# Performance work log

Measured on AMD Instinct MI355X. Metric: run time of the kernel, lower is better.

The kernel has to match this reference:

```python
import jax, jax.numpy as jnp
import numpy as np

PIECES = 64  # self.plane


def _proj(f, w1, b1, w2, b2):
    # Projection: fc2(relu(fc1(f))), final_relu=False
    h = jax.nn.relu(f @ w1 + b1)
    return h @ w2 + b2


def _cf(img, param, pieces):
    # img: [B,3,H,W], param: [B,3,P]
    # total[b,c,h,w] = sum_i clamp(img - i/P, 0, 1/P) * param[b,c,i], then * P / sum_i param
    grid = jnp.arange(pieces, dtype=img.dtype) / pieces            # [P]
    clipped = jnp.clip(img[..., None] - grid, 0.0, 1.0 / pieces)   # [B,3,H,W,P]
    total = jnp.einsum('bchwp,bcp->bchw', clipped, param)
    norm = pieces / (jnp.sum(param, axis=-1) + 1e-30)              # [B,3]
    return total * norm[:, :, None, None]


def setup_inputs() -> dict:
    key = jax.random.key(0)
    ks = jax.random.split(key, 11)
    B, H, W = 8, 256, 256
    s = 0.05
    return {
        'x': jax.random.uniform(ks[0], (B, 3, H, W), jnp.float32),
        'f_feature': jax.random.normal(ks[1], (B, 512), jnp.float32),
        'b_feature': jax.random.normal(ks[2], (B, 512), jnp.float32),
        # stacked weights for [fc_f_1, fc_b_1, fc_f_s, fc_b_s]
        'proj_w1': jax.random.normal(ks[3], (4, 512, 192), jnp.float32) * s,
        'proj_b1': jax.random.normal(ks[4], (4, 192), jnp.float32) * s,
        'proj_w2': jax.random.normal(ks[5], (4, 192, 192), jnp.float32) * s,
        'proj_b2': jax.random.normal(ks[6], (4, 192), jnp.float32) * s,
        'fc_w1': jax.random.normal(ks[7], (576, 192), jnp.float32) * s,
        'fc_b1': jax.random.normal(ks[8], (192,), jnp.float32) * s,
        'fc_w2': jax.random.normal(ks[9], (192, 192), jnp.float32) * s,
        'fc_b2': jax.random.normal(ks[10], (192,), jnp.float32) * s,
    }


def reference(x, f_feature, b_feature, proj_w1, proj_b1, proj_w2, proj_b2,
              fc_w1, fc_b1, fc_w2, fc_b2):
    B = x.shape[0]
    # rgb_to_grayscale with 3 output channels (ITU-R 601 weights)
    gw = jnp.array([0.299, 0.587, 0.114], dtype=x.dtype)
    gray = jnp.broadcast_to(jnp.einsum('bchw,c->bhw', x, gw)[:, None], x.shape)

    # four stacked Projections: inputs [f, b, f, b]
    feats = jnp.stack([f_feature, b_feature, f_feature, b_feature])       # [4,B,512]
    h = jax.nn.relu(jnp.einsum('kbi,kio->kbo', feats, proj_w1) + proj_b1[:, None, :])
    outs = jnp.einsum('kbo,koq->kbq', h, proj_w2) + proj_b2[:, None, :]   # [4,B,192]
    param_f, param_b = outs[0], outs[1]
    param_s = outs[2] + outs[3]

    cat = jnp.concatenate([param_f, param_b, param_s], axis=1)            # [B,576]
    param = _proj(cat, fc_w1, fc_b1, fc_w2, fc_b2)                        # [B,192]

    p_all = param.reshape(B, 3, PIECES)
    p_f = param_f.reshape(B, 3, PIECES)
    p_b = param_b.reshape(B, 3, PIECES)

    return (_cf(x, p_all, PIECES), _cf(gray, p_f, PIECES), _cf(gray, p_b, PIECES))
```

## Files before the change

### kernel.cpp

```cpp
#include <hip/hip_runtime.h>

#define HWSZ 65536
#define PLANE (3 * HWSZ)
#define OUTSTRIDE (8 * PLANE)
#define MAGIC 0x13572468

__global__ __launch_bounds__(384) void k_fused(
    const float* __restrict__ f, const float* __restrict__ bf,
    const float* __restrict__ pw1, const float* __restrict__ pb1,
    const float* __restrict__ pw2, const float* __restrict__ pb2,
    const float* __restrict__ fw1, const float* __restrict__ fb1,
    const float* __restrict__ fw2, const float* __restrict__ fb2,
    const float* __restrict__ x, float* __restrict__ out,
    float* __restrict__ ws) {
  __shared__ float smem[2304];
  int t = threadIdx.x, blk = blockIdx.x;

  float* outs  = ws;
  float* param = ws + 6144;
  int* flags = (int*)(ws + 8192);

  if (blk < 32) {
    int k = blk >> 3, b = blk & 7;
    int q = t % 48, s = t / 48;
    float* sf  = smem;
    float* red = smem + 512;
    float* sh  = smem + 2048;

    const float* feat = ((k & 1) ? bf : f) + b * 512;
    for (int i = t; i < 512; i += 384) sf[i] = feat[i];
    __syncthreads();

    {
      const float4* w = (const float4*)(pw1 + (size_t)k * (512 * 192));
      float4 acc = {0.f, 0.f, 0.f, 0.f};
      int i0 = s * 64;
      for (int r = 0; r < 4; ++r) {
        float4 wv[16];
#pragma unroll
        for (int j = 0; j < 16; ++j)
          wv[j] = w[(size_t)(i0 + r * 16 + j) * 48 + q];
#pragma unroll
        for (int j = 0; j < 16; ++j) {
          float v = sf[i0 + r * 16 + j];
          acc.x = fmaf(v, wv[j].x, acc.x); acc.y = fmaf(v, wv[j].y, acc.y);
          acc.z = fmaf(v, wv[j].z, acc.z); acc.w = fmaf(v, wv[j].w, acc.w);
        }
      }
      ((float4*)(red + s * 192))[q] = acc;
    }
    __syncthreads();
    if (t < 192) {
      float a = pb1[k * 192 + t];
#pragma unroll
      for (int s2 = 0; s2 < 8; ++s2) a += red[s2 * 192 + t];
      sh[t] = fmaxf(a, 0.f);
    }
    __syncthreads();
    {
      const float4* w = (const float4*)(pw2 + (size_t)k * (192 * 192));
      float4 acc = {0.f, 0.f, 0.f, 0.f};
      int i0 = s * 24;
      for (int r = 0; r < 2; ++r) {
        float4 wv[12];
#pragma unroll
        for (int j = 0; j < 12; ++j)
          wv[j] = w[(size_t)(i0 + r * 12 + j) * 48 + q];
#pragma unroll
        for (int j = 0; j < 12; ++j) {
          float v = sh[i0 + r * 12 + j];
          acc.x = fmaf(v, wv[j].x, acc.x); acc.y = fmaf(v, wv[j].y, acc.y);
          acc.z = fmaf(v, wv[j].z, acc.z); acc.w = fmaf(v, wv[j].w, acc.w);
        }
      }
      ((float4*)(red + s * 192))[q] = acc;
    }
    __syncthreads();
    if (t < 192) {
      float a = pb2[k * 192 + t];
#pragma unroll
      for (int s2 = 0; s2 < 8; ++s2) a += red[s2 * 192 + t];
      outs[(k * 8 + b) * 192 + t] = a;
    }
    __syncthreads();
    if (t == 0) {
      __threadfence();
      atomicExch(&flags[(k * 8 + b) * 16], MAGIC);
    }

    if (blk >= 8) return;

    int b2_ = blk;
    if (t < 4) {
      while (atomicAdd(&flags[(t * 8 + b2_) * 16], 0) != MAGIC)
        __builtin_amdgcn_s_sleep(2);
    }
    __syncthreads();
    if (t == 0) __threadfence();
    __syncthreads();

    float* sc   = smem;
    float* redb = smem + 576;
    float* shb  = smem + 2112;
    for (int idx = t; idx < 576; idx += 384) {
      float v;
      if (idx < 192)      v = outs[(0 * 8 + b2_) * 192 + idx];
      else if (idx < 384) v = outs[(1 * 8 + b2_) * 192 + (idx - 192)];
      else                v = outs[(2 * 8 + b2_) * 192 + (idx - 384)] +
                              outs[(3 * 8 + b2_) * 192 + (idx - 384)];
      sc[idx] = v;
    }
    __syncthreads();
    {
      int q = t % 48, s = t / 48;
      {
        const float4* w = (const float4*)fw1;
        float4 acc = {0.f, 0.f, 0.f, 0.f};
        int i0 = s * 72;
        for (int r = 0; r < 4; ++r) {
          float4 wv[18];
#pragma unroll
          for (int j = 0; j < 18; ++j)
            wv[j] = w[(size_t)(i0 + r * 18 + j) * 48 + q];
#pragma unroll
          for (int j = 0; j < 18; ++j) {
            float v = sc[i0 + r * 18 + j];
            acc.x = fmaf(v, wv[j].x, acc.x); acc.y = fmaf(v, wv[j].y, acc.y);
            acc.z = fmaf(v, wv[j].z, acc.z); acc.w = fmaf(v, wv[j].w, acc.w);
          }
        }
        ((float4*)(redb + s * 192))[q] = acc;
      }
      __syncthreads();
      if (t < 192) {
        float a = fb1[t];
#pragma unroll
        for (int s2 = 0; s2 < 8; ++s2) a += redb[s2 * 192 + t];
        shb[t] = fmaxf(a, 0.f);
      }
      __syncthreads();
      {
        const float4* w = (const float4*)fw2;
        float4 acc = {0.f, 0.f, 0.f, 0.f};
        int i0 = s * 24;
        for (int r = 0; r < 2; ++r) {
          float4 wv[12];
#pragma unroll
          for (int j = 0; j < 12; ++j)
            wv[j] = w[(size_t)(i0 + r * 12 + j) * 48 + q];
#pragma unroll
          for (int j = 0; j < 12; ++j) {
            float v = shb[i0 + r * 12 + j];
            acc.x = fmaf(v, wv[j].x, acc.x); acc.y = fmaf(v, wv[j].y, acc.y);
            acc.z = fmaf(v, wv[j].z, acc.z); acc.w = fmaf(v, wv[j].w, acc.w);
          }
        }
        ((float4*)(redb + s * 192))[q] = acc;
      }
      __syncthreads();
      if (t < 192) {
        float a = fb2[t];
#pragma unroll
        for (int s2 = 0; s2 < 8; ++s2) a += redb[s2 * 192 + t];
        param[b2_ * 192 + t] = a;
      }
    }
    __syncthreads();
    if (t == 0) {
      __threadfence();
      atomicExch(&flags[(32 + b2_) * 16], MAGIC);
    }
    return;
  }

  int rblk = blk - 32;
  int b = rblk / 43, chunk = rblk - b * 43;
  int s4 = chunk * 384 + t;
  bool act = s4 < (HWSZ / 4);

  const float* xb = x + (size_t)b * PLANE;
  float4 vr = {0,0,0,0}, vg = {0,0,0,0}, vb = {0,0,0,0};
  if (act) {
    vr = ((const float4*)(xb))[s4];
    vg = ((const float4*)(xb + HWSZ))[s4];
    vb = ((const float4*)(xb + 2 * HWSZ))[s4];
  }

  if (t == 0) {
    while (atomicAdd(&flags[(32 + b) * 16], 0) != MAGIC)
      __builtin_amdgcn_s_sleep(2);
    __threadfence();
  }
  __syncthreads();

  float2* tab = (float2*)smem;
  {
    int wave = t >> 6, lane = t & 63;
    for (int cur = wave; cur < 9; cur += 6) {
      int oi = cur / 3, c = cur - oi * 3;
      const float* src = (oi == 0) ? param + b * 192 + c * 64
                                   : outs + ((oi - 1) * 8 + b) * 192 + c * 64;
      float p = src[lane];
      float v = p;
#pragma unroll
      for (int d = 1; d < 64; d <<= 1) {
        float n = __shfl_up(v, d, 64);
        if (lane >= d) v += n;
      }
      float total = __shfl(v, 63, 64);
      float norm = 64.f / (total + 1e-30f);
      tab[cur * 64 + lane] = make_float2((v - p) * 0.015625f * norm, p * norm);
    }
  }
  __syncthreads();

  if (!act) return;

  auto ev = [&](int cur, float v) -> float {
    int k = (int)(v * 64.f);
    k = k < 0 ? 0 : (k > 63 ? 63 : k);
    float2 e = tab[cur * 64 + k];
    float tt = v - (float)k * 0.015625f;
    return fmaf(tt, e.y, e.x);
  };
  auto ev4 = [&](int cur, float4 v) -> float4 {
    float4 r;
    r.x = ev(cur, v.x); r.y = ev(cur, v.y);
    r.z = ev(cur, v.z); r.w = ev(cur, v.w);
    return r;
  };

  float4 gr;
  gr.x = fmaf(0.299f, vr.x, fmaf(0.587f, vg.x, 0.114f * vb.x));
  gr.y = fmaf(0.299f, vr.y, fmaf(0.587f, vg.y, 0.114f * vb.y));
  gr.z = fmaf(0.299f, vr.z, fmaf(0.587f, vg.z, 0.114f * vb.z));
  gr.w = fmaf(0.299f, vr.w, fmaf(0.587f, vg.w, 0.114f * vb.w));

  float* o0 = out + (size_t)b * PLANE;
  float* o1 = out + OUTSTRIDE + (size_t)b * PLANE;
  float* o2 = out + 2 * OUTSTRIDE + (size_t)b * PLANE;

  ((float4*)(o0))[s4]            = ev4(0, vr);
  ((float4*)(o0 + HWSZ))[s4]     = ev4(1, vg);
  ((float4*)(o0 + 2 * HWSZ))[s4] = ev4(2, vb);
  ((float4*)(o1))[s4]            = ev4(3, gr);
  ((float4*)(o1 + HWSZ))[s4]     = ev4(4, gr);
  ((float4*)(o1 + 2 * HWSZ))[s4] = ev4(5, gr);
  ((float4*)(o2))[s4]            = ev4(6, gr);
  ((float4*)(o2 + HWSZ))[s4]     = ev4(7, gr);
  ((float4*)(o2 + 2 * HWSZ))[s4] = ev4(8, gr);
}

extern "C" void kernel_launch(void* const* d_in, const int* in_sizes, int n_in,
                              void* d_out, int out_size, void* d_ws, size_t ws_size,
                              hipStream_t stream) {
  const float* x   = (const float*)d_in[0];
  const float* f   = (const float*)d_in[1];
  const float* bf  = (const float*)d_in[2];
  const float* pw1 = (const float*)d_in[3];
  const float* pb1 = (const float*)d_in[4];
  const float* pw2 = (const float*)d_in[5];
  const float* pb2 = (const float*)d_in[6];
  const float* fw1 = (const float*)d_in[7];
  const float* fb1 = (const float*)d_in[8];
  const float* fw2 = (const float*)d_in[9];
  const float* fb2 = (const float*)d_in[10];
  float* out = (float*)d_out;
  float* ws  = (float*)d_ws;

  k_fused<<<376, 384, 0, stream>>>(f, bf, pw1, pb1, pw2, pb2, fw1, fb1, fw2,
                                   fb2, x, out, ws);
}
```

Before: 108.6 us.

## Split fused kernel into MLP kernel and separate render kernel

The single persistent kernel is split in two. The first computes the projection MLPs (32 blocks, keeping the intra-kernel flag wait for the final fc stage), and the second renders the curve outputs over a 64x8 grid of 256-thread blocks. This removes the spin-wait of render blocks on the per-batch param flags and relies on stream ordering instead. In exchange it adds a second launch, and the loads of x can no longer overlap with the MLP computation.

```diff
diff --git a/kernel.cpp b/kernel.cpp
--- a/kernel.cpp
+++ b/kernel.cpp
@@ -5,13 +5,12 @@
 #define OUTSTRIDE (8 * PLANE)
 #define MAGIC 0x13572468
 
-__global__ __launch_bounds__(384) void k_fused(
+__global__ __launch_bounds__(384) void k_mlp(
     const float* __restrict__ f, const float* __restrict__ bf,
     const float* __restrict__ pw1, const float* __restrict__ pb1,
     const float* __restrict__ pw2, const float* __restrict__ pb2,
     const float* __restrict__ fw1, const float* __restrict__ fb1,
     const float* __restrict__ fw2, const float* __restrict__ fb2,
-    const float* __restrict__ x, float* __restrict__ out,
     float* __restrict__ ws) {
   __shared__ float smem[2304];
   int t = threadIdx.x, blk = blockIdx.x;
@@ -20,9 +19,9 @@
   float* param = ws + 6144;
   int* flags = (int*)(ws + 8192);
 
-  if (blk < 32) {
-    int k = blk >> 3, b = blk & 7;
-    int q = t % 48, s = t / 48;
+  int k = blk >> 3, b = blk & 7;
+  int q = t % 48, s = t / 48;
+  {
     float* sf  = smem;
     float* red = smem + 512;
     float* sh  = smem + 2048;
@@ -87,134 +86,109 @@
       __threadfence();
       atomicExch(&flags[(k * 8 + b) * 16], MAGIC);
     }
-
-    if (blk >= 8) return;
-
-    int b2_ = blk;
-    if (t < 4) {
-      while (atomicAdd(&flags[(t * 8 + b2_) * 16], 0) != MAGIC)
-        __builtin_amdgcn_s_sleep(2);
-    }
-    __syncthreads();
-    if (t == 0) __threadfence();
-    __syncthreads();
-
-    float* sc   = smem;
-    float* redb = smem + 576;
-    float* shb  = smem + 2112;
-    for (int idx = t; idx < 576; idx += 384) {
-      float v;
-      if (idx < 192)      v = outs[(0 * 8 + b2_) * 192 + idx];
-      else if (idx < 384) v = outs[(1 * 8 + b2_) * 192 + (idx - 192)];
-      else                v = outs[(2 * 8 + b2_) * 192 + (idx - 384)] +
-                              outs[(3 * 8 + b2_) * 192 + (idx - 384)];
-      sc[idx] = v;
-    }
-    __syncthreads();
-    {
-      int q = t % 48, s = t / 48;
-      {
-        const float4* w = (const float4*)fw1;
-        float4 acc = {0.f, 0.f, 0.f, 0.f};
-        int i0 = s * 72;
-        for (int r = 0; r < 4; ++r) {
-          float4 wv[18];
-#pragma unroll
-          for (int j = 0; j < 18; ++j)
-            wv[j] = w[(size_t)(i0 + r * 18 + j) * 48 + q];
-#pragma unroll
-          for (int j = 0; j < 18; ++j) {
-            float v = sc[i0 + r * 18 + j];
-            acc.x = fmaf(v, wv[j].x, acc.x); acc.y = fmaf(v, wv[j].y, acc.y);
-            acc.z = fmaf(v, wv[j].z, acc.z); acc.w = fmaf(v, wv[j].w, acc.w);
-          }
-        }
-        ((float4*)(redb + s * 192))[q] = acc;
-      }
-      __syncthreads();
-      if (t < 192) {
-        float a = fb1[t];
-#pragma unroll
-        for (int s2 = 0; s2 < 8; ++s2) a += redb[s2 * 192 + t];
-        shb[t] = fmaxf(a, 0.f);
-      }
-      __syncthreads();
-      {
-        const float4* w = (const float4*)fw2;
-        float4 acc = {0.f, 0.f, 0.f, 0.f};
-        int i0 = s * 24;
-        for (int r = 0; r < 2; ++r) {
-          float4 wv[12];
-#pragma unroll
-          for (int j = 0; j < 12; ++j)
-            wv[j] = w[(size_t)(i0 + r * 12 + j) * 48 + q];
-#pragma unroll
-          for (int j = 0; j < 12; ++j) {
-            float v = shb[i0 + r * 12 + j];
-            acc.x = fmaf(v, wv[j].x, acc.x); acc.y = fmaf(v, wv[j].y, acc.y);
-            acc.z = fmaf(v, wv[j].z, acc.z); acc.w = fmaf(v, wv[j].w, acc.w);
-          }
-        }
-        ((float4*)(redb + s * 192))[q] = acc;
-      }
-      __syncthreads();
-      if (t < 192) {
-        float a = fb2[t];
-#pragma unroll
-        for (int s2 = 0; s2 < 8; ++s2) a += redb[s2 * 192 + t];
-        param[b2_ * 192 + t] = a;
-      }
-    }
-    __syncthreads();
-    if (t == 0) {
-      __threadfence();
-      atomicExch(&flags[(32 + b2_) * 16], MAGIC);
-    }
-    return;
-  }
-
-  int rblk = blk - 32;
-  int b = rblk / 43, chunk = rblk - b * 43;
-  int s4 = chunk * 384 + t;
-  bool act = s4 < (HWSZ / 4);
-
-  const float* xb = x + (size_t)b * PLANE;
-  float4 vr = {0,0,0,0}, vg = {0,0,0,0}, vb = {0,0,0,0};
-  if (act) {
-    vr = ((const float4*)(xb))[s4];
-    vg = ((const float4*)(xb + HWSZ))[s4];
-    vb = ((const float4*)(xb + 2 * HWSZ))[s4];
-  }
-
-  if (t == 0) {
-    while (atomicAdd(&flags[(32 + b) * 16], 0) != MAGIC)
+  }
+
+  if (blk >= 8) return;
+
+  int b2 = blk;
+  if (t < 4) {
+    while (atomicAdd(&flags[(t * 8 + b2) * 16], 0) != MAGIC)
       __builtin_amdgcn_s_sleep(2);
-    __threadfence();
-  }
-  __syncthreads();
-
-  float2* tab = (float2*)smem;
+  }
+  __syncthreads();
+  if (t == 0) __threadfence();
+  __syncthreads();
+
+  float* sc   = smem;
+  float* redb = smem + 576;
+  float* shb  = smem + 2112;
+  for (int idx = t; idx < 576; idx += 384) {
+    float v;
+    if (idx < 192)      v = outs[(0 * 8 + b2) * 192 + idx];
+    else if (idx < 384) v = outs[(1 * 8 + b2) * 192 + (idx - 192)];
+    else                v = outs[(2 * 8 + b2) * 192 + (idx - 384)] +
+                            outs[(3 * 8 + b2) * 192 + (idx - 384)];
+    sc[idx] = v;
+  }
+  __syncthreads();
   {
-    int wave = t >> 6, lane = t & 63;
-    for (int cur = wave; cur < 9; cur += 6) {
-      int oi = cur / 3, c = cur - oi * 3;
-      const float* src = (oi == 0) ? param + b * 192 + c * 64
-                                   : outs + ((oi - 1) * 8 + b) * 192 + c * 64;
-      float p = src[lane];
-      float v = p;
-#pragma unroll
-      for (int d = 1; d < 64; d <<= 1) {
-        float n = __shfl_up(v, d, 64);
-        if (lane >= d) v += n;
-      }
-      float total = __shfl(v, 63, 64);
-      float norm = 64.f / (total + 1e-30f);
-      tab[cur * 64 + lane] = make_float2((v - p) * 0.015625f * norm, p * norm);
-    }
-  }
-  __syncthreads();
-
-  if (!act) return;
+    const float4* w = (const float4*)fw1;
+    float4 acc = {0.f, 0.f, 0.f, 0.f};
+    int i0 = s * 72;
+    for (int r = 0; r < 4; ++r) {
+      float4 wv[18];
+#pragma unroll
+      for (int j = 0; j < 18; ++j)
+        wv[j] = w[(size_t)(i0 + r * 18 + j) * 48 + q];
+#pragma unroll
+      for (int j = 0; j < 18; ++j) {
+        float v = sc[i0 + r * 18 + j];
+        acc.x = fmaf(v, wv[j].x, acc.x); acc.y = fmaf(v, wv[j].y, acc.y);
+        acc.z = fmaf(v, wv[j].z, acc.z); acc.w = fmaf(v, wv[j].w, acc.w);
+      }
+    }
+    ((float4*)(redb + s * 192))[q] = acc;
+  }
+  __syncthreads();
+  if (t < 192) {
+    float a = fb1[t];
+#pragma unroll
+    for (int s2 = 0; s2 < 8; ++s2) a += redb[s2 * 192 + t];
+    shb[t] = fmaxf(a, 0.f);
+  }
+  __syncthreads();
+  {
+    const float4* w = (const float4*)fw2;
+    float4 acc = {0.f, 0.f, 0.f, 0.f};
+    int i0 = s * 24;
+    for (int r = 0; r < 2; ++r) {
+      float4 wv[12];
+#pragma unroll
+      for (int j = 0; j < 12; ++j)
+        wv[j] = w[(size_t)(i0 + r * 12 + j) * 48 + q];
+#pragma unroll
+      for (int j = 0; j < 12; ++j) {
+        float v = shb[i0 + r * 12 + j];
+        acc.x = fmaf(v, wv[j].x, acc.x); acc.y = fmaf(v, wv[j].y, acc.y);
+        acc.z = fmaf(v, wv[j].z, acc.z); acc.w = fmaf(v, wv[j].w, acc.w);
+      }
+    }
+    ((float4*)(redb + s * 192))[q] = acc;
+  }
+  __syncthreads();
+  if (t < 192) {
+    float a = fb2[t];
+#pragma unroll
+    for (int s2 = 0; s2 < 8; ++s2) a += redb[s2 * 192 + t];
+    param[b2 * 192 + t] = a;
+  }
+}
+
+__global__ __launch_bounds__(256) void k_render(
+    const float* __restrict__ x, const float* __restrict__ ws,
+    float* __restrict__ out) {
+  int b = blockIdx.y, t = threadIdx.x;
+  int wave = t >> 6, lane = t & 63;
+  const float* outs  = ws;
+  const float* param = ws + 6144;
+  __shared__ float2 tab[576];
+
+  for (int cur = wave; cur < 9; cur += 4) {
+    int oi = cur / 3, c = cur - oi * 3;
+    const float* src = (oi == 0) ? param + b * 192 + c * 64
+                                 : outs + ((oi - 1) * 8 + b) * 192 + c * 64;
+    float p = src[lane];
+    float v = p;
+#pragma unroll
+    for (int d = 1; d < 64; d <<= 1) {
+      float n = __shfl_up(v, d, 64);
+      if (lane >= d) v += n;
+    }
+    float total = __shfl(v, 63, 64);
+    float norm = 64.f / (total + 1e-30f);
+    tab[cur * 64 + lane] = make_float2((v - p) * 0.015625f * norm, p * norm);
+  }
+  __syncthreads();
 
   auto ev = [&](int cur, float v) -> float {
     int k = (int)(v * 64.f);
@@ -229,6 +203,12 @@
     r.z = ev(cur, v.z); r.w = ev(cur, v.w);
     return r;
   };
+
+  int s4 = blockIdx.x * 256 + t;
+  const float* xb = x + (size_t)b * PLANE;
+  float4 vr = ((const float4*)(xb))[s4];
+  float4 vg = ((const float4*)(xb + HWSZ))[s4];
+  float4 vb = ((const float4*)(xb + 2 * HWSZ))[s4];
 
   float4 gr;
   gr.x = fmaf(0.299f, vr.x, fmaf(0.587f, vg.x, 0.114f * vb.x));
@@ -268,6 +248,8 @@
   float* out = (float*)d_out;
   float* ws  = (float*)d_ws;
 
-  k_fused<<<376, 384, 0, stream>>>(f, bf, pw1, pb1, pw2, pb2, fw1, fb1, fw2,
-                                   fb2, x, out, ws);
+  k_mlp<<<32, 384, 0, stream>>>(f, bf, pw1, pb1, pw2, pb2, fw1, fb1, fw2,
+                                fb2, ws);
+  dim3 grid(64, 8);
+  k_render<<<grid, 256, 0, stream>>>(x, ws, out);
 }
```

After: 101.8 us. 1.07x faster.
